# Performance work log

Hardware: AMD Instinct MI355X
Metric: run time of the kernel (lower is better)

Reference implementation:

```python
import jax, jax.numpy as jnp
import numpy as np

K = 5          # kernel size (hard-coded in feature_propogate)
DIL = 2        # dilation
PAD = (K + (DIL - 1) * (K - 1)) // 2  # = 4, same-padding for unfold


def _unfold_w_center(x):
    """torch F.unfold(kernel=5, dilation=2, padding=4) reshaped to [B,C,25,H,W].
    Neighbor index n is kernel row-major (ki*5+kj), matching torch unfold."""
    B, C, H, W = x.shape
    p = jnp.pad(x, ((0, 0), (0, 0), (PAD, PAD), (PAD, PAD)))
    nb = jnp.stack(
        [p[:, :, DIL * i: DIL * i + H, DIL * j: DIL * j + W]
         for i in range(K) for j in range(K)],
        axis=2,
    )  # [B, C, 25, H, W]
    return nb


def setup_inputs() -> dict:
    key = jax.random.key(0)
    k1, k2 = jax.random.split(key)
    feat = jax.random.normal(k1, (4, 128, 128, 128), dtype=jnp.float32) * 0.1
    w_cls = jax.random.normal(k2, (1, 128), dtype=jnp.float32) * 0.1
    b_cls = jnp.zeros((1,), dtype=jnp.float32)
    return {"feat": feat, "w_cls": w_cls, "b_cls": b_cls}


def reference(feat, w_cls, b_cls):
    # feature_propogate: unfold-based local self-attention over 5x5 dilated nbhd
    nb = _unfold_w_center(feat)                          # [B,C,25,H,W]
    corr = jnp.einsum('bchw,bcnhw->bhwn', feat, nb)      # correlation
    attn = jax.nn.softmax(jnp.maximum(corr, 0.0), -1)    # clamp(min=0) + softmax
    prop = jnp.einsum('bcnhw,bhwn->bchw', nb, attn)      # weighted gather-sum
    # 1x1 classifier (Conv2d(C, num_classes, 1))
    logits = jnp.einsum('bchw,oc->bohw', prop, w_cls) + b_cls[None, :, None, None]
    return logits
```

## Files before the change

kernel.cpp:

```cpp
#include <hip/hip_runtime.h>

#define C 128
#define H 128
#define W 128
#define HW (H*W)

__global__ __launch_bounds__(640, 5) void fused_kernel(
    const float* __restrict__ feat, const float* __restrict__ wc,
    const float* __restrict__ bc, float* __restrict__ out)
{
    __shared__ float corr_s[2][25][W];
    __shared__ float g_s[2][5][W];
    __shared__ float wc_s[C];

    const int blk0 = blockIdx.x;
    const int blk  = (blk0 & 7) * 64 + (blk0 >> 3);
    const int b    = blk >> 7;
    const int r    = blk & 127;
    const int tid  = threadIdx.x;
    const int wv   = tid >> 6;
    const int ti   = wv >> 1;
    const int h    = wv & 1;
    const int lane = tid & 63;
    const int s    = lane >> 5;
    const int pg   = lane & 31;
    const int w0   = pg * 4;

    if (tid < C) wc_s[tid] = wc[tid];
    __syncthreads();

    const int  rt  = r - 4 + 2 * ti;
    const bool rok = (unsigned)rt < (unsigned)H;

    float acc[5][4];
    float ga[4];
#pragma unroll
    for (int j = 0; j < 5; ++j)
#pragma unroll
        for (int p = 0; p < 4; ++p) acc[j][p] = 0.f;
#pragma unroll
    for (int p = 0; p < 4; ++p) ga[p] = 0.f;

    if (rok) {
        const float* fbase = feat + ((size_t)(b * C + h * 64 + s * 32)) * HW;
        const float* tp = fbase + rt * W + w0;
        const float* cp = fbase + r  * W + w0;
        const int wci = h * 64 + s * 32;
        const bool isCtr = (ti == 2);

#pragma unroll 1
        for (int cc = 0; cc < 32; cc += 4) {
            float4 T[4], D[4];
#pragma unroll
            for (int u = 0; u < 4; ++u)
                T[u] = *(const float4*)(tp + (cc + u) * HW);
            if (isCtr) {
#pragma unroll
                for (int u = 0; u < 4; ++u) D[u] = T[u];
            } else {
#pragma unroll
                for (int u = 0; u < 4; ++u)
                    D[u] = *(const float4*)(cp + (cc + u) * HW);
            }
#pragma unroll
            for (int u = 0; u < 4; ++u) {
                const float wcv = wc_s[wci + cc + u];
                const float ctr[4] = {D[u].x, D[u].y, D[u].z, D[u].w};
                float win[12];
                win[4] = T[u].x; win[5] = T[u].y; win[6] = T[u].z; win[7] = T[u].w;
                win[0]  = __shfl_up(T[u].x, 1);
                win[1]  = __shfl_up(T[u].y, 1);
                win[2]  = __shfl_up(T[u].z, 1);
                win[3]  = __shfl_up(T[u].w, 1);
                win[8]  = __shfl_down(T[u].x, 1);
                win[9]  = __shfl_down(T[u].y, 1);
                win[10] = __shfl_down(T[u].z, 1);
                win[11] = __shfl_down(T[u].w, 1);
#pragma unroll
                for (int p = 0; p < 4; ++p)
                    ga[p] = fmaf(wcv, win[4 + p], ga[p]);
#pragma unroll
                for (int p = 0; p < 4; ++p)
                    acc[2][p] = fmaf(ctr[p], win[4 + p], acc[2][p]);
#pragma unroll
                for (int j = 0; j < 5; ++j) {
                    if (j == 2) continue;
#pragma unroll
                    for (int p = 0; p < 4; ++p)
                        acc[j][p] = fmaf(ctr[p], win[p + 2 * j], acc[j][p]);
                }
            }
        }
    }

#pragma unroll
    for (int j = 0; j < 5; ++j)
#pragma unroll
        for (int p = 0; p < 4; ++p)
            acc[j][p] += __shfl_xor(acc[j][p], 32);
#pragma unroll
    for (int p = 0; p < 4; ++p) ga[p] += __shfl_xor(ga[p], 32);

    if (s == 0) {
#pragma unroll
        for (int j = 0; j < 5; ++j)
#pragma unroll
            for (int p = 0; p < 4; ++p) {
                const int  col = w0 + p - 4 + 2 * j;
                const bool ok  = rok && ((unsigned)col < (unsigned)W);
                corr_s[h][ti * 5 + j][w0 + p] = ok ? acc[j][p] : 0.f;
            }
#pragma unroll
        for (int p = 0; p < 4; ++p) g_s[h][ti][w0 + p] = ga[p];
    }
    __syncthreads();

    if (tid < W) {
        const int w = tid;
        float v[25], m = 0.f;
#pragma unroll
        for (int n = 0; n < 25; ++n) {
            v[n] = fmaxf(corr_s[0][n][w] + corr_s[1][n][w], 0.f);
            m = fmaxf(m, v[n]);
        }
        float sum = 0.f, num = 0.f;
#pragma unroll
        for (int i = 0; i < 5; ++i) {
            const bool riv = (unsigned)(r - 4 + 2 * i) < (unsigned)H;
#pragma unroll
            for (int j = 0; j < 5; ++j) {
                const float e = __expf(v[i * 5 + j] - m);
                sum += e;
                const int  wt = w - 4 + 2 * j;
                const bool ok = riv && ((unsigned)wt < (unsigned)W);
                const int  wi = ok ? wt : 0;
                const float gv = g_s[0][i][wi] + g_s[1][i][wi];
                num = fmaf(e, ok ? gv : 0.f, num);
            }
        }
        out[((size_t)(b * H + r)) * W + w] = num / sum + bc[0];
    }
}

extern "C" void kernel_launch(void* const* d_in, const int* in_sizes, int n_in,
                              void* d_out, int out_size, void* d_ws, size_t ws_size,
                              hipStream_t stream) {
    const float* feat = (const float*)d_in[0];
    const float* wcls = (const float*)d_in[1];
    const float* bcls = (const float*)d_in[2];
    float* outp = (float*)d_out;

    fused_kernel<<<dim3(4 * H), dim3(640), 0, stream>>>(feat, wcls, bcls, outp);
}
```

Measured before the change: 96.40 us.

## Pre-transpose features to row-major [B,H,C,W] layout before fused attention kernel

```diff
diff --git a/kernel.cpp b/kernel.cpp
--- a/kernel.cpp
+++ b/kernel.cpp
@@ -5,8 +5,27 @@
 #define W 128
 #define HW (H*W)
 
+__global__ __launch_bounds__(512) void transpose_kernel(
+    const float* __restrict__ feat, float* __restrict__ T)
+{
+    const int blk  = blockIdx.x;
+    const int b    = blk >> 7;
+    const int r    = blk & 127;
+    const int tid  = threadIdx.x;
+    const int wv   = tid >> 6;
+    const int lane = tid & 63;
+    const int q    = lane & 31;
+    const int ch0  = wv * 2 + (lane >> 5);
+#pragma unroll
+    for (int k = 0; k < 8; ++k) {
+        const int c = k * 16 + ch0;
+        const float4 v = *(const float4*)(feat + ((size_t)(b * C + c) * H + r) * W + q * 4);
+        *(float4*)(T + ((size_t)(b * H + r) * C + c) * W + q * 4) = v;
+    }
+}
+
 __global__ __launch_bounds__(640, 5) void fused_kernel(
-    const float* __restrict__ feat, const float* __restrict__ wc,
+    const float* __restrict__ T, const float* __restrict__ wc,
     const float* __restrict__ bc, float* __restrict__ out)
 {
     __shared__ float corr_s[2][25][W];
@@ -42,40 +61,39 @@
     for (int p = 0; p < 4; ++p) ga[p] = 0.f;
 
     if (rok) {
-        const float* fbase = feat + ((size_t)(b * C + h * 64 + s * 32)) * HW;
-        const float* tp = fbase + rt * W + w0;
-        const float* cp = fbase + r  * W + w0;
-        const int wci = h * 64 + s * 32;
+        const int cbase = h * 64 + s * 32;
+        const float* tp = T + ((size_t)(b * H + rt) * C + cbase) * W + w0;
+        const float* cp = T + ((size_t)(b * H + r ) * C + cbase) * W + w0;
         const bool isCtr = (ti == 2);
 
 #pragma unroll 1
         for (int cc = 0; cc < 32; cc += 4) {
-            float4 T[4], D[4];
+            float4 Tv[4], Dv[4];
 #pragma unroll
             for (int u = 0; u < 4; ++u)
-                T[u] = *(const float4*)(tp + (cc + u) * HW);
+                Tv[u] = *(const float4*)(tp + (cc + u) * W);
             if (isCtr) {
 #pragma unroll
-                for (int u = 0; u < 4; ++u) D[u] = T[u];
+                for (int u = 0; u < 4; ++u) Dv[u] = Tv[u];
             } else {
 #pragma unroll
                 for (int u = 0; u < 4; ++u)
-                    D[u] = *(const float4*)(cp + (cc + u) * HW);
+                    Dv[u] = *(const float4*)(cp + (cc + u) * W);
             }
 #pragma unroll
             for (int u = 0; u < 4; ++u) {
-                const float wcv = wc_s[wci + cc + u];
-                const float ctr[4] = {D[u].x, D[u].y, D[u].z, D[u].w};
+                const float wcv = wc_s[cbase + cc + u];
+                const float ctr[4] = {Dv[u].x, Dv[u].y, Dv[u].z, Dv[u].w};
                 float win[12];
-                win[4] = T[u].x; win[5] = T[u].y; win[6] = T[u].z; win[7] = T[u].w;
-                win[0]  = __shfl_up(T[u].x, 1);
-                win[1]  = __shfl_up(T[u].y, 1);
-                win[2]  = __shfl_up(T[u].z, 1);
-                win[3]  = __shfl_up(T[u].w, 1);
-                win[8]  = __shfl_down(T[u].x, 1);
-                win[9]  = __shfl_down(T[u].y, 1);
-                win[10] = __shfl_down(T[u].z, 1);
-                win[11] = __shfl_down(T[u].w, 1);
+                win[4] = Tv[u].x; win[5] = Tv[u].y; win[6] = Tv[u].z; win[7] = Tv[u].w;
+                win[0]  = __shfl_up(Tv[u].x, 1);
+                win[1]  = __shfl_up(Tv[u].y, 1);
+                win[2]  = __shfl_up(Tv[u].z, 1);
+                win[3]  = __shfl_up(Tv[u].w, 1);
+                win[8]  = __shfl_down(Tv[u].x, 1);
+                win[9]  = __shfl_down(Tv[u].y, 1);
+                win[10] = __shfl_down(Tv[u].z, 1);
+                win[11] = __shfl_down(Tv[u].w, 1);
 #pragma unroll
                 for (int p = 0; p < 4; ++p)
                     ga[p] = fmaf(wcv, win[4 + p], ga[p]);
@@ -149,6 +167,8 @@
     const float* wcls = (const float*)d_in[1];
     const float* bcls = (const float*)d_in[2];
     float* outp = (float*)d_out;
+    float* T    = (float*)d_ws;
 
-    fused_kernel<<<dim3(4 * H), dim3(640), 0, stream>>>(feat, wcls, bcls, outp);
+    transpose_kernel<<<dim3(4 * H), dim3(512), 0, stream>>>(feat, T);
+    fused_kernel<<<dim3(4 * H), dim3(640), 0, stream>>>(T, wcls, bcls, outp);
 }
```

Measured after the change: 109.1 us. +13.2%, slower.
